# Kernel tuning notes

Hardware: AMD Instinct MI355X
Metric: run time of the kernel (lower is better)

The kernel has to match this reference:

```python
import jax, jax.numpy as jnp
import numpy as np

KS = 3          # kernel_size
PAD = KS // 2   # =1, symmetric pad (pd=2, pdr=1 in the original)


def setup_inputs() -> dict:
    key = jax.random.key(0)
    k1, k2 = jax.random.split(key)
    B, H, W, T, C = 1, 48, 48, 48, 32
    q = jax.random.normal(k1, (B, H, W, T, C), dtype=jnp.float32)
    k = jax.random.normal(k2, (B, H, W, T, C), dtype=jnp.float32)
    return {"q": q, "k": k}


def reference(q, k):
    # q, k: [B, H, W, T, C]
    B, H, W, T, C = q.shape
    # zero-pad k spatially by 1 on each side (matches nnf.pad with pdr=1)
    kp = jnp.pad(k, ((0, 0), (PAD, PAD), (PAD, PAD), (PAD, PAD), (0, 0)))
    # gather the 27 shifted windows; token order (dh major, dt minor) matches
    # unfold(1).unfold(2).unfold(3) + permute in the original.
    wins = jnp.stack(
        [kp[:, a:a + H, b:b + W, c:c + T, :]
         for a in range(KS) for b in range(KS) for c in range(KS)],
        axis=4,
    )  # [B, H, W, T, 27, C]
    # QK^T over channel dim -> [B, H, W, T, 27]
    scores = jnp.einsum('bhwtc,bhwtjc->bhwtj', q, wins)
    attn = jax.nn.softmax(scores, axis=-1)
    # fixed displacement grid v: offsets (-1,0,1)^3 in (dh, dw, dt) order
    ax = jnp.arange(-(KS // 2), KS // 2 + 1, dtype=q.dtype)  # [-1, 0, 1]
    offs = jnp.stack(jnp.meshgrid(ax, ax, ax, indexing='ij'), axis=-1)
    offs = offs.reshape(KS ** 3, 3)  # [27, 3]
    # displacement-weighted sum -> [B, H, W, T, 3]
    x = jnp.einsum('bhwtj,jd->bhwtd', attn, offs)
    # -> [B, 3, H, W, T]
    return jnp.transpose(x, (0, 4, 1, 2, 3))
```

## Files before the change

kernel.cpp:

```cpp
#include <hip/hip_runtime.h>
#include <hip/hip_bf16.h>
#include <math.h>

#define DH 48
#define DW 48
#define DT 48
#define DC 32
#define NPOS (DH * DW * DT)

#define TH 2
#define TW 4
#define TT 4
#define LH (TH + 2)
#define LW (TW + 2)
#define LT (TT + 2)
#define NLINES (LH * LW * LT)
#define NF4 (NLINES * 8)
#define NTHREADS 256

typedef __attribute__((address_space(3))) unsigned int lds_u32_t;
typedef const __attribute__((address_space(1))) unsigned int glb_u32_t;

__global__ __launch_bounds__(NTHREADS, 4) void cotr_natt_kernel(
    const float* __restrict__ q,
    const float* __restrict__ k,
    float* __restrict__ out)
{
    __shared__ __align__(16) float kl[NF4 * 4];

    const int bt = blockIdx.x % (DT / TT);
    const int bw = (blockIdx.x / (DT / TT)) % (DW / TW);
    const int bh = blockIdx.x / ((DT / TT) * (DW / TW));
    const int h0 = bh * TH, w0 = bw * TW, t0 = bt * TT;

    const int tid = threadIdx.x;

#pragma unroll
    for (int i = 0; i < 5; ++i) {
        const int s = i * NTHREADS + tid;
        if (s < NF4) {
            const int line = s >> 3, c4 = s & 7;
            const int llt = line % LT;
            const int llw = (line / LT) % LW;
            const int llh = line / (LT * LW);
            const int hh = min(max(h0 + llh - 1, 0), DH - 1);
            const int ww = min(max(w0 + llw - 1, 0), DW - 1);
            const int tt = min(max(t0 + llt - 1, 0), DT - 1);
            const float* gp =
                k + ((size_t)(hh * DW + ww) * DT + tt) * DC + c4 * 4;
            __builtin_amdgcn_global_load_lds((glb_u32_t*)gp,
                                             (lds_u32_t*)&kl[s * 4], 16, 0, 0);
        }
    }

    const int p = tid >> 3;
    const int sub = tid & 7;
    const int lh = p >> 4;
    const int lw = (p >> 2) & 3;
    const int lt = p & 3;
    const int h = h0 + lh, w = w0 + lw, t = t0 + lt;
    const int idx = (h * DW + w) * DT + t;

    const float4 qv =
        *reinterpret_cast<const float4*>(q + (size_t)idx * DC + sub * 4);

    __syncthreads();

    float part[27];
#pragma unroll
    for (int a = 0; a < 3; ++a) {
#pragma unroll
        for (int b = 0; b < 3; ++b) {
#pragma unroll
            for (int c = 0; c < 3; ++c) {
                const int line = ((lh + a) * LW + (lw + b)) * LT + (lt + c);
                const float4 kv = *reinterpret_cast<const float4*>(
                    &kl[line * DC + sub * 4]);
                part[(a * 3 + b) * 3 + c] =
                    fmaf(qv.x, kv.x,
                    fmaf(qv.y, kv.y,
                    fmaf(qv.z, kv.z, qv.w * kv.w)));
            }
        }
    }

    float as_[3], bs_[3], cs_[3];
#pragma unroll
    for (int u = 0; u < 3; ++u) {
        as_[u] = ((unsigned)(h + u - 1) < DH) ? 1.0f : 0.0f;
        bs_[u] = ((unsigned)(w + u - 1) < DW) ? 1.0f : 0.0f;
        cs_[u] = ((unsigned)(t + u - 1) < DT) ? 1.0f : 0.0f;
    }

    float m = -INFINITY;
#pragma unroll
    for (int j = 0; j < 27; ++j) {
        float v = part[j];
        v += __shfl_xor(v, 1, 64);
        v += __shfl_xor(v, 2, 64);
        v += __shfl_xor(v, 4, 64);
        v *= as_[j / 9] * bs_[(j / 3) % 3] * cs_[j % 3];
        part[j] = v;
        m = fmaxf(m, v);
    }

    float sum = 0.0f;
    float oh = 0.0f, ow = 0.0f, ot = 0.0f;
#pragma unroll
    for (int j = 0; j < 27; ++j) {
        const float e = __expf(part[j] - m);
        sum += e;
        const float da = (float)(j / 9 - 1);
        const float db = (float)((j / 3) % 3 - 1);
        const float dc = (float)(j % 3 - 1);
        oh = fmaf(e, da, oh);
        ow = fmaf(e, db, ow);
        ot = fmaf(e, dc, ot);
    }
    const float inv = 1.0f / sum;

    if (sub == 0)      out[0 * NPOS + idx] = oh * inv;
    else if (sub == 1) out[1 * NPOS + idx] = ow * inv;
    else if (sub == 2) out[2 * NPOS + idx] = ot * inv;
}

extern "C" void kernel_launch(void* const* d_in, const int* in_sizes, int n_in,
                              void* d_out, int out_size, void* d_ws, size_t ws_size,
                              hipStream_t stream) {
    const float* q = reinterpret_cast<const float*>(d_in[0]);
    const float* k = reinterpret_cast<const float*>(d_in[1]);
    float* out = reinterpret_cast<float*>(d_out);

    const int blocks = (DH / TH) * (DW / TW) * (DT / TT);
    cotr_natt_kernel<<<blocks, NTHREADS, 0, stream>>>(q, k, out);
}
```

Baseline: 86.35 us.

## Use 4 lanes per position with DPP reductions and taller spatial tile

```diff
diff --git a/kernel.cpp b/kernel.cpp
--- a/kernel.cpp
+++ b/kernel.cpp
@@ -8,7 +8,7 @@
 #define DC 32
 #define NPOS (DH * DW * DT)
 
-#define TH 2
+#define TH 4
 #define TW 4
 #define TT 4
 #define LH (TH + 2)
@@ -21,7 +21,14 @@
 typedef __attribute__((address_space(3))) unsigned int lds_u32_t;
 typedef const __attribute__((address_space(1))) unsigned int glb_u32_t;
 
-__global__ __launch_bounds__(NTHREADS, 4) void cotr_natt_kernel(
+template <int CTRL>
+__device__ __forceinline__ float qperm_add(float v) {
+    const int s = __builtin_amdgcn_update_dpp(
+        0, __float_as_int(v), CTRL, 0xF, 0xF, true);
+    return v + __int_as_float(s);
+}
+
+__global__ __launch_bounds__(NTHREADS, 5) void cotr_natt_kernel(
     const float* __restrict__ q,
     const float* __restrict__ k,
     float* __restrict__ out)
@@ -36,13 +43,14 @@
     const int tid = threadIdx.x;
 
 #pragma unroll
-    for (int i = 0; i < 5; ++i) {
+    for (int i = 0; i < 7; ++i) {
         const int s = i * NTHREADS + tid;
         if (s < NF4) {
             const int line = s >> 3, c4 = s & 7;
             const int llt = line % LT;
-            const int llw = (line / LT) % LW;
-            const int llh = line / (LT * LW);
+            const int lhw = line / LT;
+            const int llw = lhw % LW;
+            const int llh = lhw / LW;
             const int hh = min(max(h0 + llh - 1, 0), DH - 1);
             const int ww = min(max(w0 + llw - 1, 0), DW - 1);
             const int tt = min(max(t0 + llt - 1, 0), DT - 1);
@@ -53,16 +61,17 @@
         }
     }
 
-    const int p = tid >> 3;
-    const int sub = tid & 7;
+    const int p = tid >> 2;
+    const int sub = tid & 3;
+    const int lt = p & 3;
+    const int lw = (p >> 2) & 3;
     const int lh = p >> 4;
-    const int lw = (p >> 2) & 3;
-    const int lt = p & 3;
     const int h = h0 + lh, w = w0 + lw, t = t0 + lt;
     const int idx = (h * DW + w) * DT + t;
 
-    const float4 qv =
-        *reinterpret_cast<const float4*>(q + (size_t)idx * DC + sub * 4);
+    const float4* qp = reinterpret_cast<const float4*>(q + (size_t)idx * DC);
+    const float4 qa = qp[sub * 2];
+    const float4 qb = qp[sub * 2 + 1];
 
     __syncthreads();
 
@@ -74,12 +83,18 @@
 #pragma unroll
             for (int c = 0; c < 3; ++c) {
                 const int line = ((lh + a) * LW + (lw + b)) * LT + (lt + c);
-                const float4 kv = *reinterpret_cast<const float4*>(
-                    &kl[line * DC + sub * 4]);
+                const float4* kp =
+                    reinterpret_cast<const float4*>(&kl[line * DC]);
+                const float4 ka = kp[sub * 2];
+                const float4 kb = kp[sub * 2 + 1];
                 part[(a * 3 + b) * 3 + c] =
-                    fmaf(qv.x, kv.x,
-                    fmaf(qv.y, kv.y,
-                    fmaf(qv.z, kv.z, qv.w * kv.w)));
+                    fmaf(qa.x, ka.x,
+                    fmaf(qa.y, ka.y,
+                    fmaf(qa.z, ka.z,
+                    fmaf(qa.w, ka.w,
+                    fmaf(qb.x, kb.x,
+                    fmaf(qb.y, kb.y,
+                    fmaf(qb.z, kb.z, qb.w * kb.w)))))));
             }
         }
     }
@@ -96,9 +111,8 @@
 #pragma unroll
     for (int j = 0; j < 27; ++j) {
         float v = part[j];
-        v += __shfl_xor(v, 1, 64);
-        v += __shfl_xor(v, 2, 64);
-        v += __shfl_xor(v, 4, 64);
+        v = qperm_add<0xB1>(v);
+        v = qperm_add<0x4E>(v);
         v *= as_[j / 9] * bs_[(j / 3) % 3] * cs_[j % 3];
         part[j] = v;
         m = fmaxf(m, v);
```

Measured after the change: 78.56 us. -9.0%, faster.
